# Kernel tuning notes

Hardware: AMD Instinct MI355X
Metric: run time of the kernel (lower is better)

The kernel has to match this reference:

```python
import jax, jax.numpy as jnp
import numpy as np

IMAGE_SIZE = 224
COV_HP = 1.0
SIGMA = 1.0
STEPS = 2
CUTOFF = 20.0
IMP_LO, IMP_HI = 0.5, 2.0
REL_W = 0.5
EPS = 1e-6

# Projection matrices for front/top/left views (buffer Js in the module)
JS = jnp.array([[[1, 0, 0], [0, 1, 0]],
                [[1, 0, 0], [0, 0, 1]],
                [[0, 0, 1], [0, 1, 0]]], dtype=jnp.float32)


def _blur(d, sigma):
    # d: [B,H,W]; separable Gaussian blur, 'same' padding
    r = max(1, int(3 * sigma))
    x = jnp.arange(-r, r + 1, dtype=jnp.float32)
    k = jnp.exp(-(x * x) / (2.0 * sigma * sigma))
    k = k / k.sum()
    d4 = d[:, None]  # [B,1,H,W]
    kh = k.reshape(1, 1, -1, 1)
    kw = k.reshape(1, 1, 1, -1)
    d4 = jax.lax.conv_general_dilated(d4, kh, (1, 1), [(r, r), (0, 0)],
                                      dimension_numbers=('NCHW', 'OIHW', 'NCHW'))
    d4 = jax.lax.conv_general_dilated(d4, kw, (1, 1), [(0, 0), (r, r)],
                                      dimension_numbers=('NCHW', 'OIHW', 'NCHW'))
    return d4[:, 0]


def _fill_depth_map(d, sigma, steps):
    # fill_depth_map is not defined in the source; implemented as iterative
    # Gaussian-blur hole filling (empty pixels take blurred neighborhood).
    for _ in range(steps):
        b = _blur(d, sigma)
        d = jnp.where(d > 1e-6, d, b)
    return d


def _forward(position, cov3d, opacity, importance):
    B, N, _ = position.shape
    H = W = IMAGE_SIZE
    Hh, Wh = H // 2, W // 2
    yy, xx = jnp.meshgrid(jnp.arange(Hh), jnp.arange(Wh), indexing='ij')
    grid = jnp.stack([xx, yy], axis=-1).astype(jnp.float32)  # [Hh,Wh,2]
    imp = jnp.clip(jnp.broadcast_to(importance[:, :N], (B, N)), IMP_LO, IMP_HI)
    imp = imp[:, :, None, None]
    eye3 = jnp.eye(3, dtype=cov3d.dtype)
    eye2 = jnp.eye(2, dtype=cov3d.dtype)
    maps = []
    for v in range(3):  # fixed small view loop, as in the source
        J = JS[v]  # [2,3]
        # NOTE: source mutates cov3d across the view loop; replicate that
        cov3d = (cov3d + jnp.swapaxes(cov3d, -1, -2)) * 0.5
        cov3d = cov3d + EPS * eye3
        nrm = jnp.linalg.norm(cov3d, axis=(-1, -2), keepdims=True)
        cov3d = cov3d / (nrm + EPS) * COV_HP
        cinv = jnp.linalg.inv(cov3d)                               # [B,N,3,3]
        cov2d_inv = jnp.einsum('ij,bnjk,lk->bnil', J, cinv, J)     # J C^-1 J^T
        cov2d_inv = cov2d_inv + eye2 * (EPS * 1e-4)
        proj = jnp.einsum('bnk,jk->bnj', position, J)              # [B,N,2]
        mn = proj.min(axis=1, keepdims=True)
        mx = proj.max(axis=1, keepdims=True)
        rng = mx - mn + 1e-6
        mn = mn - 0.5 * rng
        mx = mx + 0.5 * rng
        rng = mx - mn + 1e-6
        xy = jnp.clip((proj - mn) / rng * (Wh - 1), 0.0, Wh - 1)
        delta = grid[None, None] - xy[:, :, None, None, :]         # [B,N,Hh,Wh,2]
        mask_h = jnp.linalg.norm(delta, axis=-1) < CUTOFF
        mask = jnp.repeat(jnp.repeat(mask_h, 2, axis=2), 2, axis=3)
        exph = -jnp.einsum('bnhwj,bnjk,bnhwk->bnhw', delta, cov2d_inv, delta)
        exp_full = jax.image.resize(exph, (B, N, H, W), method='bilinear')
        exp_full = jnp.clip(exp_full, -20.0, 0.0)
        w = opacity[:, :, None, None] * imp * jnp.exp(exp_full)
        w = jnp.where(mask, w, 0.0)
        wmin = w.min(axis=1, keepdims=True)
        wmax = w.max(axis=1, keepdims=True)
        nw = (w - wmin) / (wmax - wmin + EPS) * REL_W + w / (w.sum(axis=1, keepdims=True) + EPS)
        dm = nw.sum(axis=1)  # [B,H,W]
        maps.append(_fill_depth_map(dm, SIGMA, STEPS))
    d = jnp.stack(maps, axis=1)  # [B,3,H,W], already 224x224 so resize is a no-op
    d = (d - d.mean()) / (jnp.std(d, ddof=1) + EPS)
    return d


def setup_inputs() -> dict:
    key = jax.random.key(0)
    k1, k2, k3 = jax.random.split(key, 3)
    B, N, MAXG = 1, 512, 1000
    return {
        'position': jax.random.normal(k1, (B, N, 3), dtype=jnp.float32),
        'cov3d': jax.random.normal(k2, (B, N, 3, 3), dtype=jnp.float32),
        'opacity': jax.random.uniform(k3, (B, N), dtype=jnp.float32),
        'importance': jnp.ones((1, MAXG), dtype=jnp.float32),
    }


def reference(position, cov3d, opacity, importance):
    return _forward(position, cov3d, opacity, importance)
```

## Files before the change

kernel.cpp:

```cpp
#include <hip/hip_runtime.h>
#include <math.h>


__device__ __forceinline__ float wave_min(float v) {
    #pragma unroll
    for (int o = 32; o >= 1; o >>= 1) v = fminf(v, __shfl_xor(v, o));
    return v;
}

__global__ __launch_bounds__(512) void splat_fused_kernel(
    const float* __restrict__ position, const float* __restrict__ cov3d,
    const float* __restrict__ opacity, const float* __restrict__ importance,
    float* __restrict__ dm) {
    __shared__ float4 lsA[512];
    __shared__ float2 lsB[512];
    __shared__ float red[8 * 6];
    __shared__ float4 pS[7][64], pMn[7][64], pMx[7][64];
    __shared__ int cnt;
    const int v = blockIdx.z;
    const int tx0 = blockIdx.x * 16, ty0 = blockIdx.y * 16;
    const int tid = threadIdx.x;
    const int lane = tid & 63, wave = tid >> 6;

    const int n = tid;
    const float p0 = position[n * 3 + 0];
    const float p1 = position[n * 3 + 1];
    const float p2 = position[n * 3 + 2];
    const float opimp = opacity[n] * fminf(fmaxf(importance[n], 0.5f), 2.0f);

    {
        float vals[6] = {p0, -p0, p1, -p1, p2, -p2};
        #pragma unroll
        for (int k = 0; k < 6; ++k) {
            float r = wave_min(vals[k]);
            if (lane == 0) red[wave * 6 + k] = r;
        }
    }
    __syncthreads();
    float mn6[6];
    #pragma unroll
    for (int k = 0; k < 6; ++k) {
        float r = red[k];
        #pragma unroll
        for (int w = 1; w < 8; ++w) r = fminf(r, red[w * 6 + k]);
        mn6[k] = r;
    }
    const float pmn[3] = {mn6[0], mn6[2], mn6[4]};
    const float pmx[3] = {-mn6[1], -mn6[3], -mn6[5]};

    float c00 = cov3d[n * 9 + 0], c01 = cov3d[n * 9 + 1], c02 = cov3d[n * 9 + 2];
    float c10 = cov3d[n * 9 + 3], c11 = cov3d[n * 9 + 4], c12 = cov3d[n * 9 + 5];
    float c20 = cov3d[n * 9 + 6], c21 = cov3d[n * 9 + 7], c22 = cov3d[n * 9 + 8];
    for (int vv = 0; vv <= v; ++vv) {
        float s01 = 0.5f * (c01 + c10);
        float s02 = 0.5f * (c02 + c20);
        float s12 = 0.5f * (c12 + c21);
        float s00 = c00 + 1e-6f;
        float s11 = c11 + 1e-6f;
        float s22 = c22 + 1e-6f;
        float nrm = sqrtf(s00 * s00 + s11 * s11 + s22 * s22 +
                          2.0f * (s01 * s01 + s02 * s02 + s12 * s12));
        float inv = 1.0f / (nrm + 1e-6f);
        c00 = s00 * inv; c11 = s11 * inv; c22 = s22 * inv;
        c01 = s01 * inv; c10 = c01; c02 = s02 * inv; c20 = c02;
        c12 = s12 * inv; c21 = c12;
    }
    float cof00 = c11 * c22 - c12 * c12;
    float cof01 = c02 * c12 - c01 * c22;
    float cof02 = c01 * c12 - c02 * c11;
    float det = c00 * cof00 + c01 * cof01 + c02 * cof02;
    float idet = 1.0f / det;
    float i00 = cof00 * idet;
    float i01 = cof01 * idet;
    float i02 = cof02 * idet;
    float i11 = (c00 * c22 - c02 * c02) * idet;
    float i12 = (c02 * c01 - c00 * c12) * idet;
    float i22 = (c00 * c11 - c01 * c01) * idet;

    float Aa, Ab, Ac, prx, pry;
    int ix, iy;
    if (v == 0)      { Aa = i00; Ab = i01; Ac = i11; prx = p0; pry = p1; ix = 0; iy = 1; }
    else if (v == 1) { Aa = i00; Ab = i02; Ac = i22; prx = p0; pry = p2; ix = 0; iy = 2; }
    else             { Aa = i22; Ab = i12; Ac = i11; prx = p2; pry = p1; ix = 2; iy = 1; }
    Aa += 1e-10f;
    Ac += 1e-10f;

    float mnx = pmn[ix], mxx = pmx[ix], mny = pmn[iy], mxy = pmx[iy];
    float rngx = mxx - mnx + 1e-6f;
    float mnx2 = mnx - 0.5f * rngx;
    float mxx2 = mxx + 0.5f * rngx;
    rngx = mxx2 - mnx2 + 1e-6f;
    float rngy = mxy - mny + 1e-6f;
    float mny2 = mny - 0.5f * rngy;
    float mxy2 = mxy + 0.5f * rngy;
    rngy = mxy2 - mny2 + 1e-6f;
    float gx = fminf(fmaxf((prx - mnx2) / rngx * 111.0f, 0.0f), 111.0f);
    float gy = fminf(fmaxf((pry - mny2) / rngy * 111.0f, 0.0f), 111.0f);

    if (tid == 0) cnt = 0;
    __syncthreads();
    {
        const float bx0 = (float)(tx0 >> 1), bx1 = (float)((tx0 + 15) >> 1);
        const float by0 = (float)(ty0 >> 1), by1 = (float)((ty0 + 15) >> 1);
        float dx = fmaxf(fmaxf(bx0 - gx, gx - bx1), 0.0f);
        float dy = fmaxf(fmaxf(by0 - gy, gy - by1), 0.0f);
        bool pass = (dx * dx + dy * dy) < 400.01f;
        unsigned long long m = __ballot(pass);
        int base = 0;
        if (lane == 0) base = atomicAdd(&cnt, __popcll(m));
        base = __shfl(base, 0);
        if (pass) {
            int slot = base + __popcll(m & ((1ull << lane) - 1ull));
            lsA[slot] = make_float4(Aa, 2.0f * Ab, Ac, opimp);
            lsB[slot] = make_float2(gx, gy);
        }
    }
    __syncthreads();
    const int len = cnt;

    const int qx = lane & 7, qy = lane >> 3;
    const int xh = (tx0 >> 1) + qx;
    const int yh = (ty0 >> 1) + qy;

    if (len == 0) {
        if (wave == 0) {
            #pragma unroll
            for (int py = 0; py < 2; ++py)
                #pragma unroll
                for (int px = 0; px < 2; ++px)
                    dm[(v * 224 + ty0 + 2 * qy + py) * 224 + tx0 + 2 * qx + px] = 0.0f;
        }
        return;
    }

    const int npad = (len + 15) & ~15;
    if (tid < npad - len) {
        lsA[len + tid] = make_float4(1.0f, 0.0f, 1.0f, 0.0f);
        lsB[len + tid] = make_float2(1e9f, 1e9f);
    }
    __syncthreads();

    float exA[2], eyA[2], VxA[2], VyA[2];
    #pragma unroll
    for (int p = 0; p < 2; ++p) {
        int xlo = xh - 1 + p; int xhi = min(xlo + 1, 111); xlo = max(xlo, 0);
        float wlo = p ? 0.75f : 0.25f, whi = 1.0f - wlo;
        exA[p] = wlo * (float)xlo + whi * (float)xhi;
        VxA[p] = wlo * whi * (float)(xhi - xlo) * (float)(xhi - xlo);
        int ylo = yh - 1 + p; int yhi2 = min(ylo + 1, 111); ylo = max(ylo, 0);
        eyA[p] = wlo * (float)ylo + whi * (float)yhi2;
        VyA[p] = wlo * whi * (float)(yhi2 - ylo) * (float)(yhi2 - ylo);
    }
    const float fxh = (float)xh, fyh = (float)yh;

    const int chunk = npad >> 3;
    const int cbeg = wave * chunk, cend = cbeg + chunk;

    float S00 = 0.f, S01 = 0.f, S10 = 0.f, S11 = 0.f;
    float mn00 = INFINITY, mn01 = INFINITY, mn10 = INFINITY, mn11 = INFINITY;
    float mx00 = -INFINITY, mx01 = -INFINITY, mx10 = -INFINITY, mx11 = -INFINITY;

    for (int i = cbeg; i < cend; i += 2) {
        float4 gA0 = lsA[i], gA1 = lsA[i + 1];
        float2 gB0 = lsB[i], gB1 = lsB[i + 1];
        #pragma unroll
        for (int u = 0; u < 2; ++u) {
            const float4 gA = u ? gA1 : gA0;
            const float2 gB = u ? gB1 : gB0;
            const float a = gA.x, b2 = gA.y, c = gA.z, op = gA.w;
            const float xx = gB.x, yy = gB.y;
            const float dxh = fxh - xx, dyh = fyh - yy;
            const bool inside = dxh * dxh + dyh * dyh < 400.0f;
            const float dx0 = exA[0] - xx, dx1 = exA[1] - xx;
            const float dy0 = eyA[0] - yy, dy1 = eyA[1] - yy;
            const float adx0 = a * dx0, adx1 = a * dx1;
            const float bdy0 = b2 * dy0, bdy1 = b2 * dy1;
            const float cdy0 = c * dy0 * dy0, cdy1 = c * dy1 * dy1;
            const float ax0 = a * VxA[0], ax1 = a * VxA[1];
            const float cy0 = c * VyA[0], cy1 = c * VyA[1];
            #pragma unroll
            for (int py = 0; py < 2; ++py) {
                const float dyp  = py ? dy1 : dy0;
                const float bdyp = py ? bdy1 : bdy0;
                const float cdyp = py ? cdy1 : cdy0;
                const float cyp  = py ? cy1 : cy0;
                #pragma unroll
                for (int px = 0; px < 2; ++px) {
                    const float dxp  = px ? dx1 : dx0;
                    const float adxp = px ? adx1 : adx0;
                    const float axp  = px ? ax1 : ax0;
                    float q = dxp * (adxp + bdyp) + cdyp;
                    float bil = -((q + axp) + cyp);
                    bil = fminf(fmaxf(bil, -20.0f), 0.0f);
                    bil = inside ? bil : -1e9f;
                    float w = op * __expf(bil);
                    if (py == 0 && px == 0) { S00 += w; mn00 = fminf(mn00, w); mx00 = fmaxf(mx00, w); }
                    if (py == 0 && px == 1) { S01 += w; mn01 = fminf(mn01, w); mx01 = fmaxf(mx01, w); }
                    if (py == 1 && px == 0) { S10 += w; mn10 = fminf(mn10, w); mx10 = fmaxf(mx10, w); }
                    if (py == 1 && px == 1) { S11 += w; mn11 = fminf(mn11, w); mx11 = fmaxf(mx11, w); }
                }
            }
        }
    }
    if (wave > 0) {
        pS[wave - 1][lane]  = make_float4(S00, S01, S10, S11);
        pMn[wave - 1][lane] = make_float4(mn00, mn01, mn10, mn11);
        pMx[wave - 1][lane] = make_float4(mx00, mx01, mx10, mx11);
    }
    __syncthreads();
    if (wave == 0) {
        #pragma unroll
        for (int k = 0; k < 7; ++k) {
            float4 s = pS[k][lane], m = pMn[k][lane], M = pMx[k][lane];
            S00 += s.x; S01 += s.y; S10 += s.z; S11 += s.w;
            mn00 = fminf(mn00, m.x); mn01 = fminf(mn01, m.y);
            mn10 = fminf(mn10, m.z); mn11 = fminf(mn11, m.w);
            mx00 = fmaxf(mx00, M.x); mx01 = fmaxf(mx01, M.y);
            mx10 = fmaxf(mx10, M.z); mx11 = fmaxf(mx11, M.w);
        }
        if (len < 512) {
            mn00 = fminf(mn00, 0.f); mn01 = fminf(mn01, 0.f);
            mn10 = fminf(mn10, 0.f); mn11 = fminf(mn11, 0.f);
            mx00 = fmaxf(mx00, 0.f); mx01 = fmaxf(mx01, 0.f);
            mx10 = fmaxf(mx10, 0.f); mx11 = fmaxf(mx11, 0.f);
        }
        float S4[4]  = {S00, S01, S10, S11};
        float mn4[4] = {mn00, mn01, mn10, mn11};
        float mx4[4] = {mx00, mx01, mx10, mx11};
        #pragma unroll
        for (int pp = 0; pp < 4; ++pp) {
            float S = S4[pp];
            float dmv = 0.5f * (S - 512.0f * mn4[pp]) / (mx4[pp] - mn4[pp] + 1e-6f)
                      + S / (S + 1e-6f);
            const int py = pp >> 1, px = pp & 1;
            dm[(v * 224 + ty0 + 2 * qy + py) * 224 + tx0 + 2 * qx + px] = dmv;
        }
    }
}

__global__ __launch_bounds__(256) void blur2_stats_kernel(
    const float* __restrict__ in, float* __restrict__ out,
    float2* __restrict__ partials) {
    __shared__ float A[28 * 29];
    __shared__ float T[28 * 29];
    __shared__ float r1[4], r2[4];
    const int v = blockIdx.z;
    const int tx0 = blockIdx.x * 16, ty0 = blockIdx.y * 16;
    const int tid = threadIdx.x;
    const float kw[7] = {0.00443305f, 0.05400558f, 0.24203623f, 0.39905030f,
                         0.24203623f, 0.05400558f, 0.00443305f};
    const float* __restrict__ chan = in + v * 224 * 224;

    for (int idx = tid; idx < 28 * 28; idx += 256) {
        int rr = idx / 28, c = idx % 28;
        int gyy = ty0 - 6 + rr, gxx = tx0 - 6 + c;
        float val = 0.0f;
        if (gyy >= 0 && gyy < 224 && gxx >= 0 && gxx < 224) val = chan[gyy * 224 + gxx];
        A[rr * 29 + c] = val;
    }
    __syncthreads();
    for (int idx = tid; idx < 22 * 28; idx += 256) {
        int rr = 3 + idx / 28, c = idx % 28;
        float s = 0.0f;
        #pragma unroll
        for (int i = 0; i < 7; ++i) s += kw[i] * A[(rr - 3 + i) * 29 + c];
        T[rr * 29 + c] = s;
    }
    __syncthreads();
    for (int idx = tid; idx < 22 * 22; idx += 256) {
        int rr = 3 + idx / 22, c = 3 + idx % 22;
        int gyy = ty0 - 6 + rr, gxx = tx0 - 6 + c;
        float s = 0.0f;
        #pragma unroll
        for (int j = 0; j < 7; ++j) s += kw[j] * T[rr * 29 + c - 3 + j];
        float ctr = A[rr * 29 + c];
        float d1 = ctr > 1e-6f ? ctr : s;
        if (gyy < 0 || gyy > 223 || gxx < 0 || gxx > 223) d1 = 0.0f;
        A[rr * 29 + c] = d1;
    }
    __syncthreads();
    for (int idx = tid; idx < 16 * 22; idx += 256) {
        int rr = 6 + idx / 22, c = 3 + idx % 22;
        float s = 0.0f;
        #pragma unroll
        for (int i = 0; i < 7; ++i) s += kw[i] * A[(rr - 3 + i) * 29 + c];
        T[rr * 29 + c] = s;
    }
    __syncthreads();
    float ls1 = 0.0f, ls2 = 0.0f;
    for (int idx = tid; idx < 16 * 16; idx += 256) {
        int rr = 6 + (idx >> 4), c = 6 + (idx & 15);
        float s = 0.0f;
        #pragma unroll
        for (int j = 0; j < 7; ++j) s += kw[j] * T[rr * 29 + c - 3 + j];
        float ctr = A[rr * 29 + c];
        float d2 = ctr > 1e-6f ? ctr : s;
        out[(v * 224 + ty0 + rr - 6) * 224 + (tx0 + c - 6)] = d2;
        ls1 += d2; ls2 += d2 * d2;
    }
    #pragma unroll
    for (int o = 32; o >= 1; o >>= 1) {
        ls1 += __shfl_xor(ls1, o);
        ls2 += __shfl_xor(ls2, o);
    }
    if ((tid & 63) == 0) { r1[tid >> 6] = ls1; r2[tid >> 6] = ls2; }
    __syncthreads();
    if (tid == 0) {
        float s1 = r1[0] + r1[1] + r1[2] + r1[3];
        float s2 = r2[0] + r2[1] + r2[2] + r2[3];
        partials[(blockIdx.z * 14 + blockIdx.y) * 14 + blockIdx.x] = make_float2(s1, s2);
    }
}

__global__ __launch_bounds__(256) void normalize_kernel(
    const float2* __restrict__ partials, float* __restrict__ out) {
    __shared__ double s1[256], s2[256];
    const int tid = threadIdx.x;
    double a = 0.0, b = 0.0;
    for (int i = tid; i < 588; i += 256) {
        float2 p = partials[i];
        a += (double)p.x; b += (double)p.y;
    }
    s1[tid] = a; s2[tid] = b;
    __syncthreads();
    for (int s = 128; s >= 1; s >>= 1) {
        if (tid < s) { s1[tid] += s1[tid + s]; s2[tid] += s2[tid + s]; }
        __syncthreads();
    }
    const double M = 150528.0;
    double mean = s1[0] / M;
    double var = (s2[0] - M * mean * mean) / (M - 1.0);
    double sd = sqrt(var > 0.0 ? var : 0.0);
    const int idx = blockIdx.x * 256 + tid;
    if (idx < 3 * 224 * 224)
        out[idx] = (out[idx] - (float)mean) / ((float)sd + 1e-6f);
}

extern "C" void kernel_launch(void* const* d_in, const int* in_sizes, int n_in,
                              void* d_out, int out_size, void* d_ws, size_t ws_size,
                              hipStream_t stream) {
    const float* position   = (const float*)d_in[0];
    const float* cov3d      = (const float*)d_in[1];
    const float* opacity    = (const float*)d_in[2];
    const float* importance = (const float*)d_in[3];
    float* out = (float*)d_out;

    float* dmA       = (float*)d_ws;
    float2* partials = (float2*)((float*)d_ws + 150528);

    hipLaunchKernelGGL(splat_fused_kernel, dim3(14, 14, 3), dim3(512), 0, stream,
                       position, cov3d, opacity, importance, dmA);
    hipLaunchKernelGGL(blur2_stats_kernel, dim3(14, 14, 3), dim3(256), 0, stream,
                       dmA, out, partials);
    hipLaunchKernelGGL(normalize_kernel, dim3(588), dim3(256), 0, stream,
                       partials, out);
}
```

Baseline: 90.57 us.

## Fuse splat, blur and normalize into one persistent kernel with grid barriers

Merges the three kernels into a single launch of 588 blocks of 256 threads that synchronise through two software grid barriers (an atomic counter with a spin-wait). Each thread now handles two Gaussians and four waves split the splat loop, halving the block size so all 588 blocks can be co-resident under launch_bounds(256,3). The block-to-tile mapping is permuted, and the normalized output is written straight from registers, which removes the separate read-modify-write normalize pass. The aim is to remove launch gaps and the global round-trip of the output. In exchange it depends on every block being resident at once to avoid deadlock, adds a memset launch, and halves splat parallelism per tile.

```diff
diff --git a/kernel.cpp b/kernel.cpp
--- a/kernel.cpp
+++ b/kernel.cpp
@@ -1,6 +1,26 @@
 #include <hip/hip_runtime.h>
 #include <math.h>
 
+
+#define NBLOCKS 588u
+
+__device__ __forceinline__ float g_ld(const float* p) {
+    return __hip_atomic_load(p, __ATOMIC_RELAXED, __HIP_MEMORY_SCOPE_AGENT);
+}
+__device__ __forceinline__ void g_st(float* p, float v) {
+    __hip_atomic_store(p, v, __ATOMIC_RELAXED, __HIP_MEMORY_SCOPE_AGENT);
+}
+
+__device__ __forceinline__ void grid_barrier(unsigned* cnt) {
+    __syncthreads();
+    if (threadIdx.x == 0) {
+        asm volatile("s_waitcnt vmcnt(0)" ::: "memory");
+        __hip_atomic_fetch_add(cnt, 1u, __ATOMIC_RELAXED, __HIP_MEMORY_SCOPE_AGENT);
+        while (__hip_atomic_load(cnt, __ATOMIC_RELAXED, __HIP_MEMORY_SCOPE_AGENT) < NBLOCKS)
+            __builtin_amdgcn_s_sleep(8);
+    }
+    __syncthreads();
+}
 
 __device__ __forceinline__ float wave_min(float v) {
     #pragma unroll
@@ -8,83 +28,70 @@
     return v;
 }
 
-__global__ __launch_bounds__(512) void splat_fused_kernel(
+struct SpS {
+    float4 lsA[512];
+    float2 lsB[512];
+    float4 pS[3][64], pMn[3][64], pMx[3][64];
+    float red[4 * 6];
+    int cnt;
+};
+struct BlS {
+    float A[28 * 29];
+    float T[28 * 29];
+    float r1[4], r2[4];
+};
+struct NmS {
+    double s1[256], s2[256];
+};
+union SmU { SpS sp; BlS bl; NmS nm; };
+
+__global__ __launch_bounds__(256, 3) void fused_all_kernel(
     const float* __restrict__ position, const float* __restrict__ cov3d,
     const float* __restrict__ opacity, const float* __restrict__ importance,
-    float* __restrict__ dm) {
-    __shared__ float4 lsA[512];
-    __shared__ float2 lsB[512];
-    __shared__ float red[8 * 6];
-    __shared__ float4 pS[7][64], pMn[7][64], pMx[7][64];
-    __shared__ int cnt;
+    float* __restrict__ dm, float2* __restrict__ partials,
+    float* __restrict__ out, unsigned* __restrict__ cnts) {
+    __shared__ SmU sm;
     const int v = blockIdx.z;
-    const int tx0 = blockIdx.x * 16, ty0 = blockIdx.y * 16;
+    const int pbx = (5 * blockIdx.x) % 14;
+    const int pby = (5 * blockIdx.y) % 14;
+    const int tx0 = pbx * 16, ty0 = pby * 16;
     const int tid = threadIdx.x;
     const int lane = tid & 63, wave = tid >> 6;
 
-    const int n = tid;
-    const float p0 = position[n * 3 + 0];
-    const float p1 = position[n * 3 + 1];
-    const float p2 = position[n * 3 + 2];
-    const float opimp = opacity[n] * fminf(fmaxf(importance[n], 0.5f), 2.0f);
-
+    float P0[3], P1[3], OP0, OP1;
     {
-        float vals[6] = {p0, -p0, p1, -p1, p2, -p2};
+        const int n0 = tid, n1 = tid + 256;
+        P0[0] = position[n0 * 3 + 0]; P0[1] = position[n0 * 3 + 1]; P0[2] = position[n0 * 3 + 2];
+        P1[0] = position[n1 * 3 + 0]; P1[1] = position[n1 * 3 + 1]; P1[2] = position[n1 * 3 + 2];
+        OP0 = opacity[n0] * fminf(fmaxf(importance[n0], 0.5f), 2.0f);
+        OP1 = opacity[n1] * fminf(fmaxf(importance[n1], 0.5f), 2.0f);
+    }
+    if (tid == 0) sm.sp.cnt = 0;
+    {
+        float vals[6] = { fminf(P0[0], P1[0]), fminf(-P0[0], -P1[0]),
+                          fminf(P0[1], P1[1]), fminf(-P0[1], -P1[1]),
+                          fminf(P0[2], P1[2]), fminf(-P0[2], -P1[2]) };
         #pragma unroll
         for (int k = 0; k < 6; ++k) {
             float r = wave_min(vals[k]);
-            if (lane == 0) red[wave * 6 + k] = r;
+            if (lane == 0) sm.sp.red[wave * 6 + k] = r;
         }
     }
     __syncthreads();
     float mn6[6];
     #pragma unroll
     for (int k = 0; k < 6; ++k) {
-        float r = red[k];
-        #pragma unroll
-        for (int w = 1; w < 8; ++w) r = fminf(r, red[w * 6 + k]);
+        float r = sm.sp.red[k];
+        #pragma unroll
+        for (int w = 1; w < 4; ++w) r = fminf(r, sm.sp.red[w * 6 + k]);
         mn6[k] = r;
     }
     const float pmn[3] = {mn6[0], mn6[2], mn6[4]};
     const float pmx[3] = {-mn6[1], -mn6[3], -mn6[5]};
-
-    float c00 = cov3d[n * 9 + 0], c01 = cov3d[n * 9 + 1], c02 = cov3d[n * 9 + 2];
-    float c10 = cov3d[n * 9 + 3], c11 = cov3d[n * 9 + 4], c12 = cov3d[n * 9 + 5];
-    float c20 = cov3d[n * 9 + 6], c21 = cov3d[n * 9 + 7], c22 = cov3d[n * 9 + 8];
-    for (int vv = 0; vv <= v; ++vv) {
-        float s01 = 0.5f * (c01 + c10);
-        float s02 = 0.5f * (c02 + c20);
-        float s12 = 0.5f * (c12 + c21);
-        float s00 = c00 + 1e-6f;
-        float s11 = c11 + 1e-6f;
-        float s22 = c22 + 1e-6f;
-        float nrm = sqrtf(s00 * s00 + s11 * s11 + s22 * s22 +
-                          2.0f * (s01 * s01 + s02 * s02 + s12 * s12));
-        float inv = 1.0f / (nrm + 1e-6f);
-        c00 = s00 * inv; c11 = s11 * inv; c22 = s22 * inv;
-        c01 = s01 * inv; c10 = c01; c02 = s02 * inv; c20 = c02;
-        c12 = s12 * inv; c21 = c12;
-    }
-    float cof00 = c11 * c22 - c12 * c12;
-    float cof01 = c02 * c12 - c01 * c22;
-    float cof02 = c01 * c12 - c02 * c11;
-    float det = c00 * cof00 + c01 * cof01 + c02 * cof02;
-    float idet = 1.0f / det;
-    float i00 = cof00 * idet;
-    float i01 = cof01 * idet;
-    float i02 = cof02 * idet;
-    float i11 = (c00 * c22 - c02 * c02) * idet;
-    float i12 = (c02 * c01 - c00 * c12) * idet;
-    float i22 = (c00 * c11 - c01 * c01) * idet;
-
-    float Aa, Ab, Ac, prx, pry;
     int ix, iy;
-    if (v == 0)      { Aa = i00; Ab = i01; Ac = i11; prx = p0; pry = p1; ix = 0; iy = 1; }
-    else if (v == 1) { Aa = i00; Ab = i02; Ac = i22; prx = p0; pry = p2; ix = 0; iy = 2; }
-    else             { Aa = i22; Ab = i12; Ac = i11; prx = p2; pry = p1; ix = 2; iy = 1; }
-    Aa += 1e-10f;
-    Ac += 1e-10f;
-
+    if (v == 0)      { ix = 0; iy = 1; }
+    else if (v == 1) { ix = 0; iy = 2; }
+    else             { ix = 2; iy = 1; }
     float mnx = pmn[ix], mxx = pmx[ix], mny = pmn[iy], mxy = pmx[iy];
     float rngx = mxx - mnx + 1e-6f;
     float mnx2 = mnx - 0.5f * rngx;
@@ -94,49 +101,77 @@
     float mny2 = mny - 0.5f * rngy;
     float mxy2 = mxy + 0.5f * rngy;
     rngy = mxy2 - mny2 + 1e-6f;
-    float gx = fminf(fmaxf((prx - mnx2) / rngx * 111.0f, 0.0f), 111.0f);
-    float gy = fminf(fmaxf((pry - mny2) / rngy * 111.0f, 0.0f), 111.0f);
-
-    if (tid == 0) cnt = 0;
-    __syncthreads();
-    {
-        const float bx0 = (float)(tx0 >> 1), bx1 = (float)((tx0 + 15) >> 1);
-        const float by0 = (float)(ty0 >> 1), by1 = (float)((ty0 + 15) >> 1);
+    const float bx0 = (float)(tx0 >> 1), bx1 = (float)((tx0 + 15) >> 1);
+    const float by0 = (float)(ty0 >> 1), by1 = (float)((ty0 + 15) >> 1);
+
+    for (int g = 0; g < 2; ++g) {
+        const int n = tid + (g << 8);
+        const float p0 = g ? P1[0] : P0[0];
+        const float p1 = g ? P1[1] : P0[1];
+        const float p2 = g ? P1[2] : P0[2];
+        const float opimp = g ? OP1 : OP0;
+        float c00 = cov3d[n * 9 + 0], c01 = cov3d[n * 9 + 1], c02 = cov3d[n * 9 + 2];
+        float c10 = cov3d[n * 9 + 3], c11 = cov3d[n * 9 + 4], c12 = cov3d[n * 9 + 5];
+        float c20 = cov3d[n * 9 + 6], c21 = cov3d[n * 9 + 7], c22 = cov3d[n * 9 + 8];
+        for (int vv = 0; vv <= v; ++vv) {
+            float s01 = 0.5f * (c01 + c10);
+            float s02 = 0.5f * (c02 + c20);
+            float s12 = 0.5f * (c12 + c21);
+            float s00 = c00 + 1e-6f;
+            float s11 = c11 + 1e-6f;
+            float s22 = c22 + 1e-6f;
+            float nrm = sqrtf(s00 * s00 + s11 * s11 + s22 * s22 +
+                              2.0f * (s01 * s01 + s02 * s02 + s12 * s12));
+            float inv = 1.0f / (nrm + 1e-6f);
+            c00 = s00 * inv; c11 = s11 * inv; c22 = s22 * inv;
+            c01 = s01 * inv; c10 = c01; c02 = s02 * inv; c20 = c02;
+            c12 = s12 * inv; c21 = c12;
+        }
+        float cof00 = c11 * c22 - c12 * c12;
+        float cof01 = c02 * c12 - c01 * c22;
+        float cof02 = c01 * c12 - c02 * c11;
+        float det = c00 * cof00 + c01 * cof01 + c02 * cof02;
+        float idet = 1.0f / det;
+        float i00 = cof00 * idet;
+        float i01 = cof01 * idet;
+        float i02 = cof02 * idet;
+        float i11 = (c00 * c22 - c02 * c02) * idet;
+        float i12 = (c02 * c01 - c00 * c12) * idet;
+        float i22 = (c00 * c11 - c01 * c01) * idet;
+
+        float Aa, Ab, Ac, prx, pry;
+        if (v == 0)      { Aa = i00; Ab = i01; Ac = i11; prx = p0; pry = p1; }
+        else if (v == 1) { Aa = i00; Ab = i02; Ac = i22; prx = p0; pry = p2; }
+        else             { Aa = i22; Ab = i12; Ac = i11; prx = p2; pry = p1; }
+        Aa += 1e-10f;
+        Ac += 1e-10f;
+        float gx = fminf(fmaxf((prx - mnx2) / rngx * 111.0f, 0.0f), 111.0f);
+        float gy = fminf(fmaxf((pry - mny2) / rngy * 111.0f, 0.0f), 111.0f);
+
         float dx = fmaxf(fmaxf(bx0 - gx, gx - bx1), 0.0f);
         float dy = fmaxf(fmaxf(by0 - gy, gy - by1), 0.0f);
         bool pass = (dx * dx + dy * dy) < 400.01f;
         unsigned long long m = __ballot(pass);
         int base = 0;
-        if (lane == 0) base = atomicAdd(&cnt, __popcll(m));
+        if (lane == 0) base = atomicAdd(&sm.sp.cnt, __popcll(m));
         base = __shfl(base, 0);
         if (pass) {
             int slot = base + __popcll(m & ((1ull << lane) - 1ull));
-            lsA[slot] = make_float4(Aa, 2.0f * Ab, Ac, opimp);
-            lsB[slot] = make_float2(gx, gy);
-        }
-    }
-    __syncthreads();
-    const int len = cnt;
+            sm.sp.lsA[slot] = make_float4(Aa, 2.0f * Ab, Ac, opimp);
+            sm.sp.lsB[slot] = make_float2(gx, gy);
+        }
+    }
+    __syncthreads();
+    const int len = sm.sp.cnt;
 
     const int qx = lane & 7, qy = lane >> 3;
     const int xh = (tx0 >> 1) + qx;
     const int yh = (ty0 >> 1) + qy;
 
-    if (len == 0) {
-        if (wave == 0) {
-            #pragma unroll
-            for (int py = 0; py < 2; ++py)
-                #pragma unroll
-                for (int px = 0; px < 2; ++px)
-                    dm[(v * 224 + ty0 + 2 * qy + py) * 224 + tx0 + 2 * qx + px] = 0.0f;
-        }
-        return;
-    }
-
     const int npad = (len + 15) & ~15;
     if (tid < npad - len) {
-        lsA[len + tid] = make_float4(1.0f, 0.0f, 1.0f, 0.0f);
-        lsB[len + tid] = make_float2(1e9f, 1e9f);
+        sm.sp.lsA[len + tid] = make_float4(1.0f, 0.0f, 1.0f, 0.0f);
+        sm.sp.lsB[len + tid] = make_float2(1e9f, 1e9f);
     }
     __syncthreads();
 
@@ -153,7 +188,7 @@
     }
     const float fxh = (float)xh, fyh = (float)yh;
 
-    const int chunk = npad >> 3;
+    const int chunk = npad >> 2;
     const int cbeg = wave * chunk, cend = cbeg + chunk;
 
     float S00 = 0.f, S01 = 0.f, S10 = 0.f, S11 = 0.f;
@@ -161,8 +196,8 @@
     float mx00 = -INFINITY, mx01 = -INFINITY, mx10 = -INFINITY, mx11 = -INFINITY;
 
     for (int i = cbeg; i < cend; i += 2) {
-        float4 gA0 = lsA[i], gA1 = lsA[i + 1];
-        float2 gB0 = lsB[i], gB1 = lsB[i + 1];
+        float4 gA0 = sm.sp.lsA[i], gA1 = sm.sp.lsA[i + 1];
+        float2 gB0 = sm.sp.lsB[i], gB1 = sm.sp.lsB[i + 1];
         #pragma unroll
         for (int u = 0; u < 2; ++u) {
             const float4 gA = u ? gA1 : gA0;
@@ -180,7 +215,6 @@
             const float cy0 = c * VyA[0], cy1 = c * VyA[1];
             #pragma unroll
             for (int py = 0; py < 2; ++py) {
-                const float dyp  = py ? dy1 : dy0;
                 const float bdyp = py ? bdy1 : bdy0;
                 const float cdyp = py ? cdy1 : cdy0;
                 const float cyp  = py ? cy1 : cy0;
@@ -203,15 +237,15 @@
         }
     }
     if (wave > 0) {
-        pS[wave - 1][lane]  = make_float4(S00, S01, S10, S11);
-        pMn[wave - 1][lane] = make_float4(mn00, mn01, mn10, mn11);
-        pMx[wave - 1][lane] = make_float4(mx00, mx01, mx10, mx11);
+        sm.sp.pS[wave - 1][lane]  = make_float4(S00, S01, S10, S11);
+        sm.sp.pMn[wave - 1][lane] = make_float4(mn00, mn01, mn10, mn11);
+        sm.sp.pMx[wave - 1][lane] = make_float4(mx00, mx01, mx10, mx11);
     }
     __syncthreads();
     if (wave == 0) {
         #pragma unroll
-        for (int k = 0; k < 7; ++k) {
-            float4 s = pS[k][lane], m = pMn[k][lane], M = pMx[k][lane];
+        for (int k = 0; k < 3; ++k) {
+            float4 s = sm.sp.pS[k][lane], m = sm.sp.pMn[k][lane], M = sm.sp.pMx[k][lane];
             S00 += s.x; S01 += s.y; S10 += s.z; S11 += s.w;
             mn00 = fminf(mn00, m.x); mn01 = fminf(mn01, m.y);
             mn10 = fminf(mn10, m.z); mn11 = fminf(mn11, m.w);
@@ -233,38 +267,30 @@
             float dmv = 0.5f * (S - 512.0f * mn4[pp]) / (mx4[pp] - mn4[pp] + 1e-6f)
                       + S / (S + 1e-6f);
             const int py = pp >> 1, px = pp & 1;
-            dm[(v * 224 + ty0 + 2 * qy + py) * 224 + tx0 + 2 * qx + px] = dmv;
-        }
-    }
-}
-
-__global__ __launch_bounds__(256) void blur2_stats_kernel(
-    const float* __restrict__ in, float* __restrict__ out,
-    float2* __restrict__ partials) {
-    __shared__ float A[28 * 29];
-    __shared__ float T[28 * 29];
-    __shared__ float r1[4], r2[4];
-    const int v = blockIdx.z;
-    const int tx0 = blockIdx.x * 16, ty0 = blockIdx.y * 16;
-    const int tid = threadIdx.x;
+            g_st(&dm[(v * 224 + ty0 + 2 * qy + py) * 224 + tx0 + 2 * qx + px], dmv);
+        }
+    }
+
+    grid_barrier(&cnts[0]);
+
     const float kw[7] = {0.00443305f, 0.05400558f, 0.24203623f, 0.39905030f,
                          0.24203623f, 0.05400558f, 0.00443305f};
-    const float* __restrict__ chan = in + v * 224 * 224;
+    const float* __restrict__ chan = dm + v * 224 * 224;
 
     for (int idx = tid; idx < 28 * 28; idx += 256) {
         int rr = idx / 28, c = idx % 28;
         int gyy = ty0 - 6 + rr, gxx = tx0 - 6 + c;
         float val = 0.0f;
-        if (gyy >= 0 && gyy < 224 && gxx >= 0 && gxx < 224) val = chan[gyy * 224 + gxx];
-        A[rr * 29 + c] = val;
+        if (gyy >= 0 && gyy < 224 && gxx >= 0 && gxx < 224) val = g_ld(chan + gyy * 224 + gxx);
+        sm.bl.A[rr * 29 + c] = val;
     }
     __syncthreads();
     for (int idx = tid; idx < 22 * 28; idx += 256) {
         int rr = 3 + idx / 28, c = idx % 28;
         float s = 0.0f;
         #pragma unroll
-        for (int i = 0; i < 7; ++i) s += kw[i] * A[(rr - 3 + i) * 29 + c];
-        T[rr * 29 + c] = s;
+        for (int i = 0; i < 7; ++i) s += kw[i] * sm.bl.A[(rr - 3 + i) * 29 + c];
+        sm.bl.T[rr * 29 + c] = s;
     }
     __syncthreads();
     for (int idx = tid; idx < 22 * 22; idx += 256) {
@@ -272,68 +298,66 @@
         int gyy = ty0 - 6 + rr, gxx = tx0 - 6 + c;
         float s = 0.0f;
         #pragma unroll
-        for (int j = 0; j < 7; ++j) s += kw[j] * T[rr * 29 + c - 3 + j];
-        float ctr = A[rr * 29 + c];
+        for (int j = 0; j < 7; ++j) s += kw[j] * sm.bl.T[rr * 29 + c - 3 + j];
+        float ctr = sm.bl.A[rr * 29 + c];
         float d1 = ctr > 1e-6f ? ctr : s;
         if (gyy < 0 || gyy > 223 || gxx < 0 || gxx > 223) d1 = 0.0f;
-        A[rr * 29 + c] = d1;
+        sm.bl.A[rr * 29 + c] = d1;
     }
     __syncthreads();
     for (int idx = tid; idx < 16 * 22; idx += 256) {
         int rr = 6 + idx / 22, c = 3 + idx % 22;
         float s = 0.0f;
         #pragma unroll
-        for (int i = 0; i < 7; ++i) s += kw[i] * A[(rr - 3 + i) * 29 + c];
-        T[rr * 29 + c] = s;
-    }
-    __syncthreads();
-    float ls1 = 0.0f, ls2 = 0.0f;
-    for (int idx = tid; idx < 16 * 16; idx += 256) {
-        int rr = 6 + (idx >> 4), c = 6 + (idx & 15);
+        for (int i = 0; i < 7; ++i) s += kw[i] * sm.bl.A[(rr - 3 + i) * 29 + c];
+        sm.bl.T[rr * 29 + c] = s;
+    }
+    __syncthreads();
+    const int rr2 = 6 + (tid >> 4), cc2 = 6 + (tid & 15);
+    float d2;
+    {
         float s = 0.0f;
         #pragma unroll
-        for (int j = 0; j < 7; ++j) s += kw[j] * T[rr * 29 + c - 3 + j];
-        float ctr = A[rr * 29 + c];
-        float d2 = ctr > 1e-6f ? ctr : s;
-        out[(v * 224 + ty0 + rr - 6) * 224 + (tx0 + c - 6)] = d2;
-        ls1 += d2; ls2 += d2 * d2;
-    }
+        for (int j = 0; j < 7; ++j) s += kw[j] * sm.bl.T[rr2 * 29 + cc2 - 3 + j];
+        float ctr = sm.bl.A[rr2 * 29 + cc2];
+        d2 = ctr > 1e-6f ? ctr : s;
+    }
+    float ls1 = d2, ls2 = d2 * d2;
     #pragma unroll
     for (int o = 32; o >= 1; o >>= 1) {
         ls1 += __shfl_xor(ls1, o);
         ls2 += __shfl_xor(ls2, o);
     }
-    if ((tid & 63) == 0) { r1[tid >> 6] = ls1; r2[tid >> 6] = ls2; }
+    if (lane == 0) { sm.bl.r1[wave] = ls1; sm.bl.r2[wave] = ls2; }
     __syncthreads();
     if (tid == 0) {
-        float s1 = r1[0] + r1[1] + r1[2] + r1[3];
-        float s2 = r2[0] + r2[1] + r2[2] + r2[3];
-        partials[(blockIdx.z * 14 + blockIdx.y) * 14 + blockIdx.x] = make_float2(s1, s2);
-    }
-}
-
-__global__ __launch_bounds__(256) void normalize_kernel(
-    const float2* __restrict__ partials, float* __restrict__ out) {
-    __shared__ double s1[256], s2[256];
-    const int tid = threadIdx.x;
+        float s1 = sm.bl.r1[0] + sm.bl.r1[1] + sm.bl.r1[2] + sm.bl.r1[3];
+        float s2 = sm.bl.r2[0] + sm.bl.r2[1] + sm.bl.r2[2] + sm.bl.r2[3];
+        float* pb = (float*)&partials[(v * 14 + pby) * 14 + pbx];
+        g_st(pb + 0, s1);
+        g_st(pb + 1, s2);
+    }
+
+    grid_barrier(&cnts[1]);
+
     double a = 0.0, b = 0.0;
+    const float* pb = (const float*)partials;
     for (int i = tid; i < 588; i += 256) {
-        float2 p = partials[i];
-        a += (double)p.x; b += (double)p.y;
-    }
-    s1[tid] = a; s2[tid] = b;
+        a += (double)g_ld(pb + 2 * i);
+        b += (double)g_ld(pb + 2 * i + 1);
+    }
+    sm.nm.s1[tid] = a; sm.nm.s2[tid] = b;
     __syncthreads();
     for (int s = 128; s >= 1; s >>= 1) {
-        if (tid < s) { s1[tid] += s1[tid + s]; s2[tid] += s2[tid + s]; }
+        if (tid < s) { sm.nm.s1[tid] += sm.nm.s1[tid + s]; sm.nm.s2[tid] += sm.nm.s2[tid + s]; }
         __syncthreads();
     }
     const double M = 150528.0;
-    double mean = s1[0] / M;
-    double var = (s2[0] - M * mean * mean) / (M - 1.0);
+    double mean = sm.nm.s1[0] / M;
+    double var = (sm.nm.s2[0] - M * mean * mean) / (M - 1.0);
     double sd = sqrt(var > 0.0 ? var : 0.0);
-    const int idx = blockIdx.x * 256 + tid;
-    if (idx < 3 * 224 * 224)
-        out[idx] = (out[idx] - (float)mean) / ((float)sd + 1e-6f);
+    out[(v * 224 + ty0 + (tid >> 4)) * 224 + tx0 + (tid & 15)] =
+        (d2 - (float)mean) / ((float)sd + 1e-6f);
 }
 
 extern "C" void kernel_launch(void* const* d_in, const int* in_sizes, int n_in,
@@ -347,11 +371,10 @@
 
     float* dmA       = (float*)d_ws;
     float2* partials = (float2*)((float*)d_ws + 150528);
-
-    hipLaunchKernelGGL(splat_fused_kernel, dim3(14, 14, 3), dim3(512), 0, stream,
-                       position, cov3d, opacity, importance, dmA);
-    hipLaunchKernelGGL(blur2_stats_kernel, dim3(14, 14, 3), dim3(256), 0, stream,
-                       dmA, out, partials);
-    hipLaunchKernelGGL(normalize_kernel, dim3(588), dim3(256), 0, stream,
-                       partials, out);
-}
+    unsigned* cnts   = (unsigned*)((float*)d_ws + 150528 + 1176);
+
+    hipMemsetAsync(cnts, 0, 2 * sizeof(unsigned), stream);
+    hipLaunchKernelGGL(fused_all_kernel, dim3(14, 14, 3), dim3(256), 0, stream,
+                       position, cov3d, opacity, importance, dmA, partials, out,
+                       cnts);
+}
```

After: 120.7 us. 1.33x slower.

## Fuse blur-stats and normalize kernels using a software grid barrier

Applied to the files above, without the earlier changes.

Merges the blur/statistics kernel and the normalize kernel into one launch. Blocks publish their partial sums with atomic stores, wait at a spin-based grid barrier, then each block reduces all partials and normalizes its own tile from registers. This removes one kernel launch and the global re-read and re-write of the output. It relies on all 588 blocks being co-resident, which launch_bounds(256,3) is meant to help with; if they are not, the barrier deadlocks. The counter is reset by the first kernel, so ordering on the stream matters.

```diff
diff --git a/kernel.cpp b/kernel.cpp
--- a/kernel.cpp
+++ b/kernel.cpp
@@ -1,6 +1,26 @@
 #include <hip/hip_runtime.h>
 #include <math.h>
 
+
+#define NBLOCKS 588u
+
+__device__ __forceinline__ float g_ld(const float* p) {
+    return __hip_atomic_load(p, __ATOMIC_RELAXED, __HIP_MEMORY_SCOPE_AGENT);
+}
+__device__ __forceinline__ void g_st(float* p, float v) {
+    __hip_atomic_store(p, v, __ATOMIC_RELAXED, __HIP_MEMORY_SCOPE_AGENT);
+}
+
+__device__ __forceinline__ void grid_barrier(unsigned* cnt) {
+    __syncthreads();
+    if (threadIdx.x == 0) {
+        asm volatile("s_waitcnt vmcnt(0)" ::: "memory");
+        __hip_atomic_fetch_add(cnt, 1u, __ATOMIC_RELAXED, __HIP_MEMORY_SCOPE_AGENT);
+        while (__hip_atomic_load(cnt, __ATOMIC_RELAXED, __HIP_MEMORY_SCOPE_AGENT) < NBLOCKS)
+            __builtin_amdgcn_s_sleep(8);
+    }
+    __syncthreads();
+}
 
 __device__ __forceinline__ float wave_min(float v) {
     #pragma unroll
@@ -11,7 +31,7 @@
 __global__ __launch_bounds__(512) void splat_fused_kernel(
     const float* __restrict__ position, const float* __restrict__ cov3d,
     const float* __restrict__ opacity, const float* __restrict__ importance,
-    float* __restrict__ dm) {
+    float* __restrict__ dm, unsigned* __restrict__ cnts) {
     __shared__ float4 lsA[512];
     __shared__ float2 lsB[512];
     __shared__ float red[8 * 6];
@@ -21,6 +41,9 @@
     const int tx0 = blockIdx.x * 16, ty0 = blockIdx.y * 16;
     const int tid = threadIdx.x;
     const int lane = tid & 63, wave = tid >> 6;
+
+    if (blockIdx.x == 0 && blockIdx.y == 0 && blockIdx.z == 0 && tid == 0)
+        cnts[0] = 0;
 
     const int n = tid;
     const float p0 = position[n * 3 + 0];
@@ -180,7 +203,6 @@
             const float cy0 = c * VyA[0], cy1 = c * VyA[1];
             #pragma unroll
             for (int py = 0; py < 2; ++py) {
-                const float dyp  = py ? dy1 : dy0;
                 const float bdyp = py ? bdy1 : bdy0;
                 const float cdyp = py ? cdy1 : cdy0;
                 const float cyp  = py ? cy1 : cy0;
@@ -238,15 +260,17 @@
     }
 }
 
-__global__ __launch_bounds__(256) void blur2_stats_kernel(
+__global__ __launch_bounds__(256, 3) void blur_norm_kernel(
     const float* __restrict__ in, float* __restrict__ out,
-    float2* __restrict__ partials) {
+    float2* __restrict__ partials, unsigned* __restrict__ cnts) {
     __shared__ float A[28 * 29];
     __shared__ float T[28 * 29];
     __shared__ float r1[4], r2[4];
+    __shared__ double s1[256], s2[256];
     const int v = blockIdx.z;
     const int tx0 = blockIdx.x * 16, ty0 = blockIdx.y * 16;
     const int tid = threadIdx.x;
+    const int lane = tid & 63, wave = tid >> 6;
     const float kw[7] = {0.00443305f, 0.05400558f, 0.24203623f, 0.39905030f,
                          0.24203623f, 0.05400558f, 0.00443305f};
     const float* __restrict__ chan = in + v * 224 * 224;
@@ -287,39 +311,38 @@
         T[rr * 29 + c] = s;
     }
     __syncthreads();
-    float ls1 = 0.0f, ls2 = 0.0f;
-    for (int idx = tid; idx < 16 * 16; idx += 256) {
-        int rr = 6 + (idx >> 4), c = 6 + (idx & 15);
+    const int rr2 = 6 + (tid >> 4), cc2 = 6 + (tid & 15);
+    float d2;
+    {
         float s = 0.0f;
         #pragma unroll
-        for (int j = 0; j < 7; ++j) s += kw[j] * T[rr * 29 + c - 3 + j];
-        float ctr = A[rr * 29 + c];
-        float d2 = ctr > 1e-6f ? ctr : s;
-        out[(v * 224 + ty0 + rr - 6) * 224 + (tx0 + c - 6)] = d2;
-        ls1 += d2; ls2 += d2 * d2;
-    }
+        for (int j = 0; j < 7; ++j) s += kw[j] * T[rr2 * 29 + cc2 - 3 + j];
+        float ctr = A[rr2 * 29 + cc2];
+        d2 = ctr > 1e-6f ? ctr : s;
+    }
+    float ls1 = d2, ls2 = d2 * d2;
     #pragma unroll
     for (int o = 32; o >= 1; o >>= 1) {
         ls1 += __shfl_xor(ls1, o);
         ls2 += __shfl_xor(ls2, o);
     }
-    if ((tid & 63) == 0) { r1[tid >> 6] = ls1; r2[tid >> 6] = ls2; }
+    if (lane == 0) { r1[wave] = ls1; r2[wave] = ls2; }
     __syncthreads();
     if (tid == 0) {
-        float s1 = r1[0] + r1[1] + r1[2] + r1[3];
-        float s2 = r2[0] + r2[1] + r2[2] + r2[3];
-        partials[(blockIdx.z * 14 + blockIdx.y) * 14 + blockIdx.x] = make_float2(s1, s2);
-    }
-}
-
-__global__ __launch_bounds__(256) void normalize_kernel(
-    const float2* __restrict__ partials, float* __restrict__ out) {
-    __shared__ double s1[256], s2[256];
-    const int tid = threadIdx.x;
+        float a = r1[0] + r1[1] + r1[2] + r1[3];
+        float b = r2[0] + r2[1] + r2[2] + r2[3];
+        float* pb = (float*)&partials[(v * 14 + blockIdx.y) * 14 + blockIdx.x];
+        g_st(pb + 0, a);
+        g_st(pb + 1, b);
+    }
+
+    grid_barrier(&cnts[0]);
+
     double a = 0.0, b = 0.0;
+    const float* pb = (const float*)partials;
     for (int i = tid; i < 588; i += 256) {
-        float2 p = partials[i];
-        a += (double)p.x; b += (double)p.y;
+        a += (double)g_ld(pb + 2 * i);
+        b += (double)g_ld(pb + 2 * i + 1);
     }
     s1[tid] = a; s2[tid] = b;
     __syncthreads();
@@ -331,9 +354,10 @@
     double mean = s1[0] / M;
     double var = (s2[0] - M * mean * mean) / (M - 1.0);
     double sd = sqrt(var > 0.0 ? var : 0.0);
-    const int idx = blockIdx.x * 256 + tid;
-    if (idx < 3 * 224 * 224)
-        out[idx] = (out[idx] - (float)mean) / ((float)sd + 1e-6f);
+    const float fmean = (float)mean;
+    const float finv = 1.0f / ((float)sd + 1e-6f);
+    out[(v * 224 + ty0 + (tid >> 4)) * 224 + tx0 + (tid & 15)] =
+        (d2 - fmean) * finv;
 }
 
 extern "C" void kernel_launch(void* const* d_in, const int* in_sizes, int n_in,
@@ -347,11 +371,10 @@
 
     float* dmA       = (float*)d_ws;
     float2* partials = (float2*)((float*)d_ws + 150528);
+    unsigned* cnts   = (unsigned*)((float*)d_ws + 150528 + 1176);
 
     hipLaunchKernelGGL(splat_fused_kernel, dim3(14, 14, 3), dim3(512), 0, stream,
-                       position, cov3d, opacity, importance, dmA);
-    hipLaunchKernelGGL(blur2_stats_kernel, dim3(14, 14, 3), dim3(256), 0, stream,
-                       dmA, out, partials);
-    hipLaunchKernelGGL(normalize_kernel, dim3(588), dim3(256), 0, stream,
-                       partials, out);
-}
+                       position, cov3d, opacity, importance, dmA, cnts);
+    hipLaunchKernelGGL(blur_norm_kernel, dim3(14, 14, 3), dim3(256), 0, stream,
+                       dmA, out, partials, cnts);
+}
```

New measurement: 106.5 us. 1.18x slower.
